# Optimization experiments

Hardware: AMD Instinct MI355X
Metric: run time of the kernel (lower is better)

The kernel has to match this reference:

```python
import jax, jax.numpy as jnp
import numpy as np

PRED_LEN = 24
F, I, H = 64, 128, 512  # features_size, input_size, hidden_size
B, S = 1024, 168        # batch, seq_len


def setup_inputs() -> dict:
    key = jax.random.key(0)
    ks = jax.random.split(key, 14)
    s = 0.05
    return {
        "x": jax.random.normal(ks[0], (B, S, F), dtype=jnp.float32),
        "W_enc": jax.random.normal(ks[1], (I, F), dtype=jnp.float32) * s,
        "b_enc": jax.random.normal(ks[2], (I,), dtype=jnp.float32) * s,
        "Wih0": jax.random.normal(ks[3], (4 * H, I), dtype=jnp.float32) * s,
        "Whh0": jax.random.normal(ks[4], (4 * H, H), dtype=jnp.float32) * s,
        "bih0": jax.random.normal(ks[5], (4 * H,), dtype=jnp.float32) * s,
        "bhh0": jax.random.normal(ks[6], (4 * H,), dtype=jnp.float32) * s,
        "Wih1": jax.random.normal(ks[7], (4 * H, H), dtype=jnp.float32) * s,
        "Whh1": jax.random.normal(ks[8], (4 * H, H), dtype=jnp.float32) * s,
        "bih1": jax.random.normal(ks[9], (4 * H,), dtype=jnp.float32) * s,
        "bhh1": jax.random.normal(ks[10], (4 * H,), dtype=jnp.float32) * s,
        "W_dec": jax.random.normal(ks[11], (F, H), dtype=jnp.float32) * s,
        "b_dec": jax.random.normal(ks[12], (F,), dtype=jnp.float32) * s,
    }


def _lstm_cell(xt, h, c, Wih, Whh, bih, bhh):
    # PyTorch gate order: i, f, g, o
    gates = xt @ Wih.T + h @ Whh.T + (bih + bhh)
    i, f, g, o = jnp.split(gates, 4, axis=-1)
    c = jax.nn.sigmoid(f) * c + jax.nn.sigmoid(i) * jnp.tanh(g)
    h = jax.nn.sigmoid(o) * jnp.tanh(c)
    return h, c


def reference(x, W_enc, b_enc, Wih0, Whh0, bih0, bhh0,
              Wih1, Whh1, bih1, bhh1, W_dec, b_dec):
    batch = x.shape[0]
    h0 = jnp.zeros((batch, H), x.dtype)
    init = (h0, h0, h0, h0)  # (h_l0, c_l0, h_l1, c_l1)

    def step(carry, xt):
        hl0, cl0, hl1, cl1 = carry
        enc = xt @ W_enc.T + b_enc
        hl0, cl0 = _lstm_cell(enc, hl0, cl0, Wih0, Whh0, bih0, bhh0)
        hl1, cl1 = _lstm_cell(hl0, hl1, cl1, Wih1, Whh1, bih1, bhh1)
        out = hl1 @ W_dec.T + b_dec
        return (hl0, cl0, hl1, cl1), out

    # teacher-forced pass over the observed sequence; keep only last output
    carry, outs = jax.lax.scan(step, init, jnp.transpose(x, (1, 0, 2)))
    last = outs[-1]  # [B, F], prediction for step seq_len (idx = seq_len-1)

    def ar_step(state, _):
        carry, prev = state
        carry, out = step(carry, prev)
        return (carry, out), out

    _, ar_outs = jax.lax.scan(ar_step, (carry, last), None, length=PRED_LEN - 1)
    outputs = jnp.concatenate([last[None], ar_outs], axis=0)  # [pred_len, B, F]
    return jnp.transpose(outputs, (1, 0, 2))  # [B, pred_len, F]
```

## Files before the change

### kernel.cpp

```cpp
#include <hip/hip_runtime.h>

#define B_   1024
#define S_   168
#define F_   64
#define I_   128
#define H_   512
#define G4   2048
#define PRED 24

typedef unsigned short u16;
typedef unsigned int   u32;
typedef __attribute__((ext_vector_type(8))) __bf16 bf16x8;
typedef __attribute__((ext_vector_type(4))) float  f32x4;
typedef __attribute__((ext_vector_type(4))) int    i32x4;

__device__ __forceinline__ u16 f2bf(float f) {
  u32 u = __float_as_uint(f);
  u += 0x7fff + ((u >> 16) & 1);
  return (u16)(u >> 16);
}
__device__ __forceinline__ float bf2f(u16 h) {
  return __uint_as_float(((u32)h) << 16);
}
__device__ __forceinline__ float sigm(float x) {
  x = fminf(fmaxf(x, -30.f), 30.f);
  return 1.f / (1.f + __expf(-x));
}
__device__ __forceinline__ float tanh_(float x) {
  x = fminf(fmaxf(x, -15.f), 15.f);
  float e = __expf(2.f * x);
  return (e - 1.f) / (e + 1.f);
}


__global__ void k_split(const float* __restrict__ src, u16* __restrict__ hi,
                        u16* __restrict__ lo, int n) {
  for (int i = blockIdx.x * 256 + threadIdx.x; i < n; i += gridDim.x * 256) {
    float a = src[i];
    u16 h = f2bf(a);
    hi[i] = h;
    lo[i] = f2bf(a - bf2f(h));
  }
}

__global__ void k_w0c(const float* __restrict__ Wih0, const float* __restrict__ Wenc,
                      float* __restrict__ W0c) {
  int id = blockIdx.x * 256 + threadIdx.x;
  int j = id >> 6, f = id & 63;
  float s = 0.f;
  for (int i = 0; i < 128; ++i) s += Wih0[j * 128 + i] * Wenc[i * 64 + f];
  W0c[id] = s;
}

__global__ void k_w0cd(const float* __restrict__ W0c, const float* __restrict__ Wdec,
                       float* __restrict__ W0cd) {
  int id = blockIdx.x * 256 + threadIdx.x;
  int j = id >> 9, m = id & 511;
  float s = 0.f;
  for (int f = 0; f < 64; ++f) s += W0c[j * 64 + f] * Wdec[f * 512 + m];
  W0cd[id] = s;
}

__global__ void k_biases(const float* __restrict__ Wih0, const float* __restrict__ benc,
                         const float* __restrict__ bih0, const float* __restrict__ bhh0,
                         const float* __restrict__ bih1, const float* __restrict__ bhh1,
                         float* __restrict__ b0c, float* __restrict__ b1c) {
  int j = blockIdx.x * 256 + threadIdx.x;
  float s = 0.f;
  for (int i = 0; i < 128; ++i) s += Wih0[j * 128 + i] * benc[i];
  b0c[j] = s + bih0[j] + bhh0[j];
  b1c[j] = bih1[j] + bhh1[j];
}

__global__ void k_b0ar(const float* __restrict__ W0c, const float* __restrict__ bdec,
                       const float* __restrict__ b0c, float* __restrict__ b0ar) {
  int j = blockIdx.x * 256 + threadIdx.x;
  float s = 0.f;
  for (int f = 0; f < 64; ++f) s += W0c[j * 64 + f] * bdec[f];
  b0ar[j] = b0c[j] + s;
}

__global__ void k_pack(const float* __restrict__ W, int K, u16* __restrict__ dst) {
  int id = blockIdx.x * 256 + threadIdx.x;
  int lane = id & 63, fi = id >> 6;
  int NK = K >> 5;
  int kt = fi % NK, jg = fi / NK;
  int g = jg & 3, jt = jg >> 2;
  int j = jt * 16 + (lane & 15);
  int kb = kt * 32 + (lane >> 4) * 8;
  const float* src = W + (size_t)(g * 512 + j) * K + kb;
  u16 hi[8] __attribute__((aligned(16)));
  u16 lo[8] __attribute__((aligned(16)));
#pragma unroll
  for (int e = 0; e < 8; ++e) {
    float v = src[e];
    u16 h = f2bf(v);
    hi[e] = h;
    lo[e] = f2bf(v - bf2f(h));
  }
  u16* d = dst + (size_t)fi * 1024 + lane * 8;
  *(i32x4*)d = *(const i32x4*)hi;
  *(i32x4*)(d + 512) = *(const i32x4*)lo;
}

__global__ __launch_bounds__(512, 2) void lstm3(
    const u16* __restrict__ A1hi, const u16* __restrict__ A1lo, int strideA1, int K1,
    const u16* __restrict__ W1p,
    const u16* __restrict__ A2hi, const u16* __restrict__ A2lo,
    const u16* __restrict__ W2p,
    const float* __restrict__ bias,
    float* __restrict__ c,
    u16* __restrict__ hhi, u16* __restrict__ hlo)
{
  __shared__ __align__(16) u16 smem_[49152];

  const int t = threadIdx.x;
  const int jblk = blockIdx.x, mblk = blockIdx.y;
  const int mbase = mblk * 64;
  const int lane = t & 63, wv = t >> 6;
  const int kk = wv >> 1, jh = wv & 1;
  const int lr = lane & 15, qk = lane >> 4;
  const int jtg = jblk * 2 + jh;
  const int nc1 = (K1 == 64) ? 1 : 4;
  const int NC  = nc1 + 4;
  const int NK1 = K1 >> 5;

  f32x4 acc[4][4];
#pragma unroll
  for (int mi = 0; mi < 4; ++mi)
#pragma unroll
    for (int g = 0; g < 4; ++g) acc[mi][g] = (f32x4){0.f, 0.f, 0.f, 0.f};

  auto prm = [&](int cc, const u16*& Ah, const u16*& Al, int& st, int& kb, int& Kc,
                 const u16*& Wp, int& NK) {
    if (cc < nc1) { Ah = A1hi; Al = A1lo; st = strideA1; kb = cc * 128;
                    Kc = (K1 == 64) ? 64 : 128; Wp = W1p; NK = NK1; }
    else { int i = cc - nc1; Ah = A2hi; Al = A2lo; st = 512; kb = i * 128;
           Kc = 128; Wp = W2p; NK = 16; }
  };
  auto nsof = [&](int cc) { return (cc < nc1 && K1 == 64) ? 2 : 4; };

  auto stageLoad = [&](int cc, i32x4* rr) {
    const u16 *Ah, *Al, *Wp_; int st, kb, Kc, NK;
    prm(cc, Ah, Al, st, kb, Kc, Wp_, NK);
    const int ppr = Kc >> 3;
    const int npc = (Kc == 128) ? 4 : 2;
#pragma unroll 4
    for (int p = 0; p < npc; ++p) {
      int li   = p * 512 + t;
      int part = li >= 64 * ppr;
      int liw  = li - part * 64 * ppr;
      int rown = (ppr == 16) ? (liw >> 4) : (liw >> 3);
      int kp   = liw & (ppr - 1);
      const u16* src = (part ? Al : Ah) + (size_t)(mbase + rown) * st + kb + kp * 8;
      rr[p] = *(const i32x4*)src;
    }
  };
  auto stageWrite = [&](int cc, const i32x4* rr, int buf) {
    const int Kc  = (cc < nc1 && K1 == 64) ? 64 : 128;
    const int ppr = Kc >> 3;
    const int npc = (Kc == 128) ? 4 : 2;
    u16* sb = smem_ + buf * 16384;
#pragma unroll 4
    for (int p = 0; p < npc; ++p) {
      int li   = p * 512 + t;
      int part = li >= 64 * ppr;
      int liw  = li - part * 64 * ppr;
      int rown = (ppr == 16) ? (liw >> 4) : (liw >> 3);
      int kp   = liw & (ppr - 1);
      *(i32x4*)&sb[(((part * 64 + rown) * ppr) + (kp ^ (rown & (ppr - 1)))) * 8] = rr[p];
    }
  };
  auto loadW = [&](const u16* Wp_, int NK, int kt, i32x4* wh, i32x4* wl) {
#pragma unroll
    for (int g = 0; g < 4; ++g) {
      const u16* p = Wp_ + (size_t)((jtg * 4 + g) * NK + kt) * 1024 + lane * 8;
      wh[g] = *(const i32x4*)p;
      wl[g] = *(const i32x4*)(p + 512);
    }
  };
  auto mstep = [&](int buf, int ppr, const i32x4* wh, const i32x4* wl) {
    const u16* sb = smem_ + buf * 16384;
    bf16x8 ah[4], al[4];
#pragma unroll
    for (int mi = 0; mi < 4; ++mi) {
      int rowA = mi * 16 + lr;
      int pl   = (kk * 4 + qk) ^ (rowA & (ppr - 1));
      ah[mi] = *(const bf16x8*)&sb[(rowA * ppr + pl) * 8];
      al[mi] = *(const bf16x8*)&sb[((64 + rowA) * ppr + pl) * 8];
    }
#pragma unroll
    for (int g = 0; g < 4; ++g) {
      bf16x8 bh = __builtin_bit_cast(bf16x8, wh[g]);
      bf16x8 bl = __builtin_bit_cast(bf16x8, wl[g]);
#pragma unroll
      for (int mi = 0; mi < 4; ++mi) {
        acc[mi][g] = __builtin_amdgcn_mfma_f32_16x16x32_bf16(ah[mi], bh, acc[mi][g], 0, 0, 0);
        acc[mi][g] = __builtin_amdgcn_mfma_f32_16x16x32_bf16(al[mi], bh, acc[mi][g], 0, 0, 0);
        acc[mi][g] = __builtin_amdgcn_mfma_f32_16x16x32_bf16(ah[mi], bl, acc[mi][g], 0, 0, 0);
      }
    }
  };

  i32x4 sreg[4];
  i32x4 whA[4], wlA[4], whB[4], wlB[4];

  stageLoad(0, sreg);
  stageWrite(0, sreg, 0);
  {
    const u16 *Ah, *Al, *Wp_; int st, kb, Kc, NK;
    prm(0, Ah, Al, st, kb, Kc, Wp_, NK);
    if (kk < nsof(0)) loadW(Wp_, NK, (kb >> 5) + kk, whA, wlA);
  }
  __syncthreads();

  for (int cc = 0; cc < NC; ++cc) {
    const int buf  = cc & 1;
    const bool more = (cc + 1 < NC);
    if (more) {
      stageLoad(cc + 1, sreg);
      const u16 *Ah, *Al, *Wp_; int st, kb, Kc, NK;
      prm(cc + 1, Ah, Al, st, kb, Kc, Wp_, NK);
      if (kk < nsof(cc + 1)) loadW(Wp_, NK, (kb >> 5) + kk, whB, wlB);
    }
    {
      const u16 *Ah, *Al, *Wp_; int st, kb, Kc, NK;
      prm(cc, Ah, Al, st, kb, Kc, Wp_, NK);
      if (kk < nsof(cc)) mstep(buf, Kc >> 3, whA, wlA);
    }
    if (more) stageWrite(cc + 1, sreg, buf ^ 1);
    __syncthreads();
    if (more) {
#pragma unroll
      for (int g = 0; g < 4; ++g) { whA[g] = whB[g]; wlA[g] = wlB[g]; }
    }
  }

  float* red = (float*)smem_;
#pragma unroll
  for (int mi = 0; mi < 4; ++mi) {
    if (mi != kk) {
      int slot = kk - (kk > mi ? 1 : 0);
      float* base = red + (size_t)(((jh * 4 + mi) * 3 + slot) * 1024) + lane * 4;
#pragma unroll
      for (int g = 0; g < 4; ++g) *(f32x4*)(base + g * 256) = acc[mi][g];
    }
  }
  __syncthreads();

  f32x4 r[4];
#pragma unroll
  for (int g = 0; g < 4; ++g) r[g] = acc[0][g];
  if (kk == 1) {
#pragma unroll
    for (int g = 0; g < 4; ++g) r[g] = acc[1][g];
  } else if (kk == 2) {
#pragma unroll
    for (int g = 0; g < 4; ++g) r[g] = acc[2][g];
  } else if (kk == 3) {
#pragma unroll
    for (int g = 0; g < 4; ++g) r[g] = acc[3][g];
  }
#pragma unroll
  for (int s = 0; s < 3; ++s) {
    float* base = red + (size_t)(((jh * 4 + kk) * 3 + s) * 1024) + lane * 4;
#pragma unroll
    for (int g = 0; g < 4; ++g) r[g] += *(const f32x4*)(base + g * 256);
  }

  const int   j   = jblk * 32 + jh * 16 + lr;
  const float bi  = bias[j];
  const float bff = bias[512 + j];
  const float bg  = bias[1024 + j];
  const float bo  = bias[1536 + j];
#pragma unroll
  for (int rr = 0; rr < 4; ++rr) {
    int b   = mbase + kk * 16 + qk * 4 + rr;
    int idx = b * 512 + j;
    float iv = sigm(r[0][rr] + bi);
    float fv = sigm(r[1][rr] + bff);
    float gv = tanh_(r[2][rr] + bg);
    float ov = sigm(r[3][rr] + bo);
    float cn = fv * c[idx] + iv * gv;
    c[idx] = cn;
    float hn = ov * tanh_(cn);
    u16 hh = f2bf(hn);
    hhi[idx] = hh;
    hlo[idx] = f2bf(hn - bf2f(hh));
  }
}

__global__ __launch_bounds__(256) void k_decoder(
    const u16* __restrict__ hhi, const u16* __restrict__ hlo,
    const float* __restrict__ Wdec, const float* __restrict__ bdec,
    float* __restrict__ out)
{
  __shared__ float sH[64][65];
  const int t = threadIdx.x;
  const int bbase = blockIdx.x * 64;
  const int mbase = blockIdx.y * 64;
  {
    int b = bbase + (t >> 2);
#pragma unroll
    for (int v = 0; v < 2; ++v) {
      int m0 = (t & 3) * 16 + v * 8;
      i32x4 hv = *(const i32x4*)&hhi[b * 512 + mbase + m0];
      i32x4 lv = *(const i32x4*)&hlo[b * 512 + mbase + m0];
      const u16* hp = (const u16*)&hv;
      const u16* lp = (const u16*)&lv;
#pragma unroll
      for (int e = 0; e < 8; ++e)
        sH[t >> 2][m0 + e] = bf2f(hp[e]) + bf2f(lp[e]);
    }
  }
  __syncthreads();
  const int bl = t & 63;
  const int wv = t >> 6;
  float acc[16];
#pragma unroll
  for (int u = 0; u < 16; ++u) acc[u] = 0.f;
  for (int m = 0; m < 64; ++m) {
    float hv = sH[bl][m];
#pragma unroll
    for (int u = 0; u < 16; ++u)
      acc[u] += hv * Wdec[(u * 4 + wv) * 512 + mbase + m];
  }
#pragma unroll
  for (int u = 0; u < 16; ++u) {
    int f = u * 4 + wv;
    float v = acc[u];
    if (blockIdx.y == 0) v += bdec[f];
    atomicAdd(&out[(bbase + bl) * (PRED * F_) + f], v);
  }
}


extern "C" void kernel_launch(void* const* d_in, const int* in_sizes, int n_in,
                              void* d_out, int out_size, void* d_ws, size_t ws_size,
                              hipStream_t stream) {
  const float* x    = (const float*)d_in[0];
  const float* Wenc = (const float*)d_in[1];
  const float* benc = (const float*)d_in[2];
  const float* Wih0 = (const float*)d_in[3];
  const float* Whh0 = (const float*)d_in[4];
  const float* bih0 = (const float*)d_in[5];
  const float* bhh0 = (const float*)d_in[6];
  const float* Wih1 = (const float*)d_in[7];
  const float* Whh1 = (const float*)d_in[8];
  const float* bih1 = (const float*)d_in[9];
  const float* bhh1 = (const float*)d_in[10];
  const float* Wdec = (const float*)d_in[11];
  const float* bdec = (const float*)d_in[12];
  float* out = (float*)d_out;

  char* p = (char*)d_ws;
  auto carve = [&](size_t bytes) { char* r = p; p += (bytes + 255) & ~(size_t)255; return r; };
  const size_t NX = (size_t)B_ * S_ * F_;
  const size_t NH = (size_t)B_ * H_;
  const size_t WP512 = (size_t)G4 * 512 * 2;
  u16* Xhi    = (u16*)carve(NX * 2);
  u16* Xlo    = (u16*)carve(NX * 2);
  float* W0c  = (float*)carve((size_t)G4 * 64 * 4);
  float* W0cd = (float*)carve((size_t)G4 * 512 * 4);
  u16* W0cp   = (u16*)carve((size_t)G4 * 64 * 2 * 2);
  u16* W0cdp  = (u16*)carve(WP512 * 2);
  u16* Whh0p  = (u16*)carve(WP512 * 2);
  u16* Wih1p  = (u16*)carve(WP512 * 2);
  u16* Whh1p  = (u16*)carve(WP512 * 2);
  float* b0c  = (float*)carve(G4 * 4);
  float* b0ar = (float*)carve(G4 * 4);
  float* b1c  = (float*)carve(G4 * 4);
  u16* h0hi[2] = {(u16*)carve(NH * 2), (u16*)carve(NH * 2)};
  u16* h0lo[2] = {(u16*)carve(NH * 2), (u16*)carve(NH * 2)};
  u16* h1hi[2] = {(u16*)carve(NH * 2), (u16*)carve(NH * 2)};
  u16* h1lo[2] = {(u16*)carve(NH * 2), (u16*)carve(NH * 2)};
  float* c0 = (float*)carve(NH * 4);
  float* c1 = (float*)carve(NH * 4);
  (void)ws_size; (void)n_in; (void)in_sizes;

  hipMemsetAsync(d_out, 0, (size_t)out_size * 4, stream);
  hipMemsetAsync(h0hi[0], 0, NH * 2, stream);
  hipMemsetAsync(h0lo[0], 0, NH * 2, stream);
  hipMemsetAsync(h1hi[0], 0, NH * 2, stream);
  hipMemsetAsync(h1lo[0], 0, NH * 2, stream);
  hipMemsetAsync(c0, 0, NH * 4, stream);
  hipMemsetAsync(c1, 0, NH * 4, stream);

  k_split<<<4096, 256, 0, stream>>>(x, Xhi, Xlo, (int)NX);
  k_w0c<<<512, 256, 0, stream>>>(Wih0, Wenc, W0c);
  k_w0cd<<<4096, 256, 0, stream>>>(W0c, Wdec, W0cd);
  k_biases<<<8, 256, 0, stream>>>(Wih0, benc, bih0, bhh0, bih1, bhh1, b0c, b1c);
  k_b0ar<<<8, 256, 0, stream>>>(W0c, bdec, b0c, b0ar);
  k_pack<<<32 * 16, 256, 0, stream>>>(Whh0, 512, Whh0p);
  k_pack<<<32 * 16, 256, 0, stream>>>(Wih1, 512, Wih1p);
  k_pack<<<32 * 16, 256, 0, stream>>>(Whh1, 512, Whh1p);
  k_pack<<<32 * 16, 256, 0, stream>>>(W0cd, 512, W0cdp);
  k_pack<<<32 * 2, 256, 0, stream>>>(W0c, 64, W0cp);

  dim3 grid(16, 16);
  for (int s = 0; s < S_ + PRED - 1; ++s) {
    int pp = s & 1, np = 1 - pp;
    if (s < S_) {
      lstm3<<<grid, 512, 0, stream>>>(
          Xhi + (size_t)s * F_, Xlo + (size_t)s * F_, S_ * F_, 64, W0cp,
          h0hi[pp], h0lo[pp], Whh0p,
          b0c, c0, h0hi[np], h0lo[np]);
    } else {
      lstm3<<<grid, 512, 0, stream>>>(
          h1hi[pp], h1lo[pp], 512, 512, W0cdp,
          h0hi[pp], h0lo[pp], Whh0p,
          b0ar, c0, h0hi[np], h0lo[np]);
    }
    lstm3<<<grid, 512, 0, stream>>>(
        h0hi[np], h0lo[np], 512, 512, Wih1p,
        h1hi[pp], h1lo[pp], Whh1p,
        b1c, c1, h1hi[np], h1lo[np]);
    if (s >= S_ - 1) {
      k_decoder<<<dim3(16, 8), 256, 0, stream>>>(
          h1hi[np], h1lo[np], Wdec, bdec, out + (size_t)(s - (S_ - 1)) * F_);
    }
  }
}
```

Measured before the change: 8.833 ms.

## Replace per-step kernel launches with a persistent cooperative LSTM kernel

Replaces the roughly 380 separate per-timestep lstm3 and decoder launches with one cooperative persistent kernel of 256 workgroups that loops over all timesteps. Grid-wide atomic-counter barriers separate the layer passes. Hidden states are interleaved as packed hi/lo bf16 pairs in u32 and read and written with agent-scope atomics, so the barriers can order them. The decoder is folded into the persistent loop. This removes launch overhead and inter-kernel gaps, at the cost of spin-barrier latency and of uncached atomic loads for the activations.

```diff
diff --git a/kernel.cpp b/kernel.cpp
--- a/kernel.cpp
+++ b/kernel.cpp
@@ -3,10 +3,11 @@
 #define B_   1024
 #define S_   168
 #define F_   64
-#define I_   128
 #define H_   512
 #define G4   2048
 #define PRED 24
+#define NWG  256
+#define NTH  512
 
 typedef unsigned short u16;
 typedef unsigned int   u32;
@@ -19,9 +20,7 @@
   u += 0x7fff + ((u >> 16) & 1);
   return (u16)(u >> 16);
 }
-__device__ __forceinline__ float bf2f(u16 h) {
-  return __uint_as_float(((u32)h) << 16);
-}
+__device__ __forceinline__ float bf2f(u16 h) { return __uint_as_float(((u32)h) << 16); }
 __device__ __forceinline__ float sigm(float x) {
   x = fminf(fmaxf(x, -30.f), 30.f);
   return 1.f / (1.f + __expf(-x));
@@ -33,13 +32,12 @@
 }
 
 
-__global__ void k_split(const float* __restrict__ src, u16* __restrict__ hi,
-                        u16* __restrict__ lo, int n) {
+__global__ void k_splitpack(const float* __restrict__ src, u32* __restrict__ dst, int n) {
   for (int i = blockIdx.x * 256 + threadIdx.x; i < n; i += gridDim.x * 256) {
     float a = src[i];
     u16 h = f2bf(a);
-    hi[i] = h;
-    lo[i] = f2bf(a - bf2f(h));
+    u16 l = f2bf(a - bf2f(h));
+    dst[i] = (u32)h | ((u32)l << 16);
   }
 }
 
@@ -103,234 +101,283 @@
   *(i32x4*)(d + 512) = *(const i32x4*)lo;
 }
 
-__global__ __launch_bounds__(512, 2) void lstm3(
-    const u16* __restrict__ A1hi, const u16* __restrict__ A1lo, int strideA1, int K1,
-    const u16* __restrict__ W1p,
-    const u16* __restrict__ A2hi, const u16* __restrict__ A2lo,
-    const u16* __restrict__ W2p,
-    const float* __restrict__ bias,
-    float* __restrict__ c,
-    u16* __restrict__ hhi, u16* __restrict__ hlo)
-{
-  __shared__ __align__(16) u16 smem_[49152];
+
+struct Params {
+  const u32* Xp;
+  const u16 *W0cp, *W0cdp, *Whh0p, *Wih1p, *Whh1p;
+  const float *b0c, *b0ar, *b1c;
+  u32 *h0a, *h0b, *h1a, *h1b;
+  float *c0, *c1;
+  const float *Wdec, *bdec;
+  float* out;
+  u32* cnt;
+};
+
+__global__ __launch_bounds__(NTH, 2) void lstm_persist(Params P) {
+  __shared__ __align__(16) u32 smem_[24576];
 
   const int t = threadIdx.x;
-  const int jblk = blockIdx.x, mblk = blockIdx.y;
+  const int wg = blockIdx.x;
+  const int jblk = wg & 15, mblk = wg >> 4;
   const int mbase = mblk * 64;
   const int lane = t & 63, wv = t >> 6;
   const int kk = wv >> 1, jh = wv & 1;
   const int lr = lane & 15, qk = lane >> 4;
   const int jtg = jblk * 2 + jh;
-  const int nc1 = (K1 == 64) ? 1 : 4;
-  const int NC  = nc1 + 4;
-  const int NK1 = K1 >> 5;
-
-  f32x4 acc[4][4];
-#pragma unroll
-  for (int mi = 0; mi < 4; ++mi)
-#pragma unroll
-    for (int g = 0; g < 4; ++g) acc[mi][g] = (f32x4){0.f, 0.f, 0.f, 0.f};
-
-  auto prm = [&](int cc, const u16*& Ah, const u16*& Al, int& st, int& kb, int& Kc,
-                 const u16*& Wp, int& NK) {
-    if (cc < nc1) { Ah = A1hi; Al = A1lo; st = strideA1; kb = cc * 128;
-                    Kc = (K1 == 64) ? 64 : 128; Wp = W1p; NK = NK1; }
-    else { int i = cc - nc1; Ah = A2hi; Al = A2lo; st = 512; kb = i * 128;
-           Kc = 128; Wp = W2p; NK = 16; }
+
+  u32 v[16];
+  i32x4 whA[4], wlA[4], whB[4], wlB[4];
+
+  auto gbar = [&](int tgt) {
+    __syncthreads();
+    if (t == 0) {
+      __hip_atomic_fetch_add(P.cnt, 1u, __ATOMIC_RELEASE, __HIP_MEMORY_SCOPE_AGENT);
+      while ((int)__hip_atomic_load(P.cnt, __ATOMIC_RELAXED, __HIP_MEMORY_SCOPE_AGENT) < tgt)
+        __builtin_amdgcn_s_sleep(1);
+    }
+    __syncthreads();
   };
-  auto nsof = [&](int cc) { return (cc < nc1 && K1 == 64) ? 2 : 4; };
-
-  auto stageLoad = [&](int cc, i32x4* rr) {
-    const u16 *Ah, *Al, *Wp_; int st, kb, Kc, NK;
-    prm(cc, Ah, Al, st, kb, Kc, Wp_, NK);
-    const int ppr = Kc >> 3;
-    const int npc = (Kc == 128) ? 4 : 2;
-#pragma unroll 4
-    for (int p = 0; p < npc; ++p) {
-      int li   = p * 512 + t;
-      int part = li >= 64 * ppr;
-      int liw  = li - part * 64 * ppr;
-      int rown = (ppr == 16) ? (liw >> 4) : (liw >> 3);
-      int kp   = liw & (ppr - 1);
-      const u16* src = (part ? Al : Ah) + (size_t)(mbase + rown) * st + kb + kp * 8;
-      rr[p] = *(const i32x4*)src;
+
+  auto layer_pass = [&](const u32* A1, int st1, int K1, const u16* W1p, bool a1u,
+                        const u32* A2, const u16* W2p,
+                        const float* bias, float* cmem, u32* hout) {
+    const int nc1 = (K1 == 64) ? 1 : 4;
+    const int NC  = nc1 + 4;
+    const int NK1 = K1 >> 5;
+
+    f32x4 acc[4][4];
+#pragma unroll
+    for (int mi = 0; mi < 4; ++mi)
+#pragma unroll
+      for (int g = 0; g < 4; ++g) acc[mi][g] = (f32x4){0.f, 0.f, 0.f, 0.f};
+
+    auto chunkKc = [&](int cc) { return (cc < nc1 && K1 == 64) ? 64 : 128; };
+    auto prmA = [&](int cc, const u32*& A, int& st, int& kb, bool& unc,
+                    const u16*& Wp, int& NK) {
+      if (cc < nc1) { A = A1; st = st1; kb = cc * 128; unc = a1u; Wp = W1p; NK = NK1; }
+      else { A = A2; st = 512; kb = (cc - nc1) * 128; unc = true; Wp = W2p; NK = 16; }
+    };
+
+    auto stage_load = [&](int cc) {
+      const u32* A; int st, kb; bool unc; const u16* Wp; int NK;
+      prmA(cc, A, st, kb, unc, Wp, NK);
+      if (chunkKc(cc) == 128) {
+        int rb = t >> 7, col = t & 127;
+        const u32* base = A + (size_t)(mbase + rb) * st + kb + col;
+        if (unc) {
+#pragma unroll
+          for (int i = 0; i < 16; ++i)
+            v[i] = __hip_atomic_load(base + (size_t)i * 4 * st, __ATOMIC_RELAXED,
+                                     __HIP_MEMORY_SCOPE_AGENT);
+        } else {
+#pragma unroll
+          for (int i = 0; i < 16; ++i) v[i] = base[(size_t)i * 4 * st];
+        }
+      } else {
+        int rb = t >> 6, col = t & 63;
+        const u32* base = A + (size_t)(mbase + rb) * st + kb + col;
+        if (unc) {
+#pragma unroll
+          for (int i = 0; i < 8; ++i)
+            v[i] = __hip_atomic_load(base + (size_t)i * 8 * st, __ATOMIC_RELAXED,
+                                     __HIP_MEMORY_SCOPE_AGENT);
+        } else {
+#pragma unroll
+          for (int i = 0; i < 8; ++i) v[i] = base[(size_t)i * 8 * st];
+        }
+      }
+    };
+
+    auto stage_write = [&](int cc, int buf) {
+      u32* sb = smem_ + buf * 8192;
+      if (chunkKc(cc) == 128) {
+        int rb = t >> 7, col = t & 127;
+        int pcol = col >> 3, e = col & 7;
+#pragma unroll
+        for (int i = 0; i < 16; ++i) {
+          int row = i * 4 + rb;
+          sb[row * 128 + (pcol ^ (row & 15)) * 8 + e] = v[i];
+        }
+      } else {
+        int rb = t >> 6, col = t & 63;
+        int pcol = col >> 3, e = col & 7;
+#pragma unroll
+        for (int i = 0; i < 8; ++i) {
+          int row = i * 8 + rb;
+          sb[row * 64 + (pcol ^ (row & 7)) * 8 + e] = v[i];
+        }
+      }
+    };
+
+    auto loadW = [&](const u16* Wp, int NK, int kt, i32x4* wh, i32x4* wl) {
+#pragma unroll
+      for (int g = 0; g < 4; ++g) {
+        const u16* p_ = Wp + (size_t)((jtg * 4 + g) * NK + kt) * 1024 + lane * 8;
+        wh[g] = *(const i32x4*)p_;
+        wl[g] = *(const i32x4*)(p_ + 512);
+      }
+    };
+
+    auto mstep = [&](int buf, int Kc) {
+      const u32* sb = smem_ + buf * 8192;
+      const int pm = (Kc >> 3) - 1;
+      bf16x8 ah[4], al[4];
+#pragma unroll
+      for (int mi = 0; mi < 4; ++mi) {
+        int rowA = mi * 16 + lr;
+        int pw = (kk * 4 + qk) ^ (rowA & pm);
+        const u32* pp_ = sb + rowA * Kc + pw * 8;
+        i32x4 d0 = *(const i32x4*)pp_;
+        i32x4 d1 = *(const i32x4*)(pp_ + 4);
+        i32x4 hv = { (int)__builtin_amdgcn_perm((u32)d0[1], (u32)d0[0], 0x05040100),
+                     (int)__builtin_amdgcn_perm((u32)d0[3], (u32)d0[2], 0x05040100),
+                     (int)__builtin_amdgcn_perm((u32)d1[1], (u32)d1[0], 0x05040100),
+                     (int)__builtin_amdgcn_perm((u32)d1[3], (u32)d1[2], 0x05040100) };
+        i32x4 lv = { (int)__builtin_amdgcn_perm((u32)d0[1], (u32)d0[0], 0x07060302),
+                     (int)__builtin_amdgcn_perm((u32)d0[3], (u32)d0[2], 0x07060302),
+                     (int)__builtin_amdgcn_perm((u32)d1[1], (u32)d1[0], 0x07060302),
+                     (int)__builtin_amdgcn_perm((u32)d1[3], (u32)d1[2], 0x07060302) };
+        ah[mi] = __builtin_bit_cast(bf16x8, hv);
+        al[mi] = __builtin_bit_cast(bf16x8, lv);
+      }
+#pragma unroll
+      for (int g = 0; g < 4; ++g) {
+        bf16x8 bh = __builtin_bit_cast(bf16x8, whA[g]);
+        bf16x8 bl = __builtin_bit_cast(bf16x8, wlA[g]);
+#pragma unroll
+        for (int mi = 0; mi < 4; ++mi) {
+          acc[mi][g] = __builtin_amdgcn_mfma_f32_16x16x32_bf16(ah[mi], bh, acc[mi][g], 0, 0, 0);
+          acc[mi][g] = __builtin_amdgcn_mfma_f32_16x16x32_bf16(al[mi], bh, acc[mi][g], 0, 0, 0);
+          acc[mi][g] = __builtin_amdgcn_mfma_f32_16x16x32_bf16(ah[mi], bl, acc[mi][g], 0, 0, 0);
+        }
+      }
+    };
+
+    stage_load(0);
+    stage_write(0, 0);
+    {
+      const u32* A; int st, kb; bool unc; const u16* Wp; int NK;
+      prmA(0, A, st, kb, unc, Wp, NK);
+      if (kk < (chunkKc(0) >> 5)) loadW(Wp, NK, (kb >> 5) + kk, whA, wlA);
+    }
+    __syncthreads();
+
+    for (int cc = 0; cc < NC; ++cc) {
+      int buf = cc & 1;
+      bool more = cc + 1 < NC;
+      if (more) {
+        stage_load(cc + 1);
+        const u32* A; int st, kb; bool unc; const u16* Wp; int NK;
+        prmA(cc + 1, A, st, kb, unc, Wp, NK);
+        if (kk < (chunkKc(cc + 1) >> 5)) loadW(Wp, NK, (kb >> 5) + kk, whB, wlB);
+      }
+      if (kk < (chunkKc(cc) >> 5)) mstep(buf, chunkKc(cc));
+      if (more) stage_write(cc + 1, buf ^ 1);
+      __syncthreads();
+      if (more) {
+#pragma unroll
+        for (int g = 0; g < 4; ++g) { whA[g] = whB[g]; wlA[g] = wlB[g]; }
+      }
+    }
+
+    float* red = (float*)smem_;
+#pragma unroll
+    for (int mi = 0; mi < 4; ++mi) {
+      if (mi != kk) {
+        int slot = kk - (kk > mi ? 1 : 0);
+        float* base = red + (size_t)(((jh * 4 + mi) * 3 + slot) * 1024) + lane * 4;
+#pragma unroll
+        for (int g = 0; g < 4; ++g) *(f32x4*)(base + g * 256) = acc[mi][g];
+      }
+    }
+    __syncthreads();
+
+    f32x4 r[4];
+#pragma unroll
+    for (int g = 0; g < 4; ++g) r[g] = acc[0][g];
+    if (kk == 1) {
+#pragma unroll
+      for (int g = 0; g < 4; ++g) r[g] = acc[1][g];
+    } else if (kk == 2) {
+#pragma unroll
+      for (int g = 0; g < 4; ++g) r[g] = acc[2][g];
+    } else if (kk == 3) {
+#pragma unroll
+      for (int g = 0; g < 4; ++g) r[g] = acc[3][g];
+    }
+#pragma unroll
+    for (int sl = 0; sl < 3; ++sl) {
+      float* base = red + (size_t)(((jh * 4 + kk) * 3 + sl) * 1024) + lane * 4;
+#pragma unroll
+      for (int g = 0; g < 4; ++g) r[g] += *(const f32x4*)(base + g * 256);
+    }
+
+    const int   j   = jblk * 32 + jh * 16 + lr;
+    const float bi  = bias[j];
+    const float bff = bias[512 + j];
+    const float bg  = bias[1024 + j];
+    const float bo  = bias[1536 + j];
+#pragma unroll
+    for (int rr = 0; rr < 4; ++rr) {
+      int b   = mbase + kk * 16 + qk * 4 + rr;
+      int idx = b * 512 + j;
+      float iv = sigm(r[0][rr] + bi);
+      float fv = sigm(r[1][rr] + bff);
+      float gv = tanh_(r[2][rr] + bg);
+      float ov = sigm(r[3][rr] + bo);
+      float cn = fv * cmem[idx] + iv * gv;
+      cmem[idx] = cn;
+      float hn = ov * tanh_(cn);
+      u16 hh = f2bf(hn);
+      u16 hl = f2bf(hn - bf2f(hh));
+      u32 hp = (u32)hh | ((u32)hl << 16);
+      __hip_atomic_store(&hout[idx], hp, __ATOMIC_RELAXED, __HIP_MEMORY_SCOPE_AGENT);
     }
   };
-  auto stageWrite = [&](int cc, const i32x4* rr, int buf) {
-    const int Kc  = (cc < nc1 && K1 == 64) ? 64 : 128;
-    const int ppr = Kc >> 3;
-    const int npc = (Kc == 128) ? 4 : 2;
-    u16* sb = smem_ + buf * 16384;
-#pragma unroll 4
-    for (int p = 0; p < npc; ++p) {
-      int li   = p * 512 + t;
-      int part = li >= 64 * ppr;
-      int liw  = li - part * 64 * ppr;
-      int rown = (ppr == 16) ? (liw >> 4) : (liw >> 3);
-      int kp   = liw & (ppr - 1);
-      *(i32x4*)&sb[(((part * 64 + rown) * ppr) + (kp ^ (rown & (ppr - 1)))) * 8] = rr[p];
-    }
-  };
-  auto loadW = [&](const u16* Wp_, int NK, int kt, i32x4* wh, i32x4* wl) {
-#pragma unroll
-    for (int g = 0; g < 4; ++g) {
-      const u16* p = Wp_ + (size_t)((jtg * 4 + g) * NK + kt) * 1024 + lane * 8;
-      wh[g] = *(const i32x4*)p;
-      wl[g] = *(const i32x4*)(p + 512);
-    }
-  };
-  auto mstep = [&](int buf, int ppr, const i32x4* wh, const i32x4* wl) {
-    const u16* sb = smem_ + buf * 16384;
-    bf16x8 ah[4], al[4];
-#pragma unroll
-    for (int mi = 0; mi < 4; ++mi) {
-      int rowA = mi * 16 + lr;
-      int pl   = (kk * 4 + qk) ^ (rowA & (ppr - 1));
-      ah[mi] = *(const bf16x8*)&sb[(rowA * ppr + pl) * 8];
-      al[mi] = *(const bf16x8*)&sb[((64 + rowA) * ppr + pl) * 8];
-    }
-#pragma unroll
-    for (int g = 0; g < 4; ++g) {
-      bf16x8 bh = __builtin_bit_cast(bf16x8, wh[g]);
-      bf16x8 bl = __builtin_bit_cast(bf16x8, wl[g]);
-#pragma unroll
-      for (int mi = 0; mi < 4; ++mi) {
-        acc[mi][g] = __builtin_amdgcn_mfma_f32_16x16x32_bf16(ah[mi], bh, acc[mi][g], 0, 0, 0);
-        acc[mi][g] = __builtin_amdgcn_mfma_f32_16x16x32_bf16(al[mi], bh, acc[mi][g], 0, 0, 0);
-        acc[mi][g] = __builtin_amdgcn_mfma_f32_16x16x32_bf16(ah[mi], bl, acc[mi][g], 0, 0, 0);
-      }
-    }
-  };
-
-  i32x4 sreg[4];
-  i32x4 whA[4], wlA[4], whB[4], wlB[4];
-
-  stageLoad(0, sreg);
-  stageWrite(0, sreg, 0);
-  {
-    const u16 *Ah, *Al, *Wp_; int st, kb, Kc, NK;
-    prm(0, Ah, Al, st, kb, Kc, Wp_, NK);
-    if (kk < nsof(0)) loadW(Wp_, NK, (kb >> 5) + kk, whA, wlA);
-  }
-  __syncthreads();
-
-  for (int cc = 0; cc < NC; ++cc) {
-    const int buf  = cc & 1;
-    const bool more = (cc + 1 < NC);
-    if (more) {
-      stageLoad(cc + 1, sreg);
-      const u16 *Ah, *Al, *Wp_; int st, kb, Kc, NK;
-      prm(cc + 1, Ah, Al, st, kb, Kc, Wp_, NK);
-      if (kk < nsof(cc + 1)) loadW(Wp_, NK, (kb >> 5) + kk, whB, wlB);
-    }
-    {
-      const u16 *Ah, *Al, *Wp_; int st, kb, Kc, NK;
-      prm(cc, Ah, Al, st, kb, Kc, Wp_, NK);
-      if (kk < nsof(cc)) mstep(buf, Kc >> 3, whA, wlA);
-    }
-    if (more) stageWrite(cc + 1, sreg, buf ^ 1);
-    __syncthreads();
-    if (more) {
-#pragma unroll
-      for (int g = 0; g < 4; ++g) { whA[g] = whB[g]; wlA[g] = wlB[g]; }
-    }
-  }
-
-  float* red = (float*)smem_;
-#pragma unroll
-  for (int mi = 0; mi < 4; ++mi) {
-    if (mi != kk) {
-      int slot = kk - (kk > mi ? 1 : 0);
-      float* base = red + (size_t)(((jh * 4 + mi) * 3 + slot) * 1024) + lane * 4;
-#pragma unroll
-      for (int g = 0; g < 4; ++g) *(f32x4*)(base + g * 256) = acc[mi][g];
-    }
-  }
-  __syncthreads();
-
-  f32x4 r[4];
-#pragma unroll
-  for (int g = 0; g < 4; ++g) r[g] = acc[0][g];
-  if (kk == 1) {
-#pragma unroll
-    for (int g = 0; g < 4; ++g) r[g] = acc[1][g];
-  } else if (kk == 2) {
-#pragma unroll
-    for (int g = 0; g < 4; ++g) r[g] = acc[2][g];
-  } else if (kk == 3) {
-#pragma unroll
-    for (int g = 0; g < 4; ++g) r[g] = acc[3][g];
-  }
-#pragma unroll
-  for (int s = 0; s < 3; ++s) {
-    float* base = red + (size_t)(((jh * 4 + kk) * 3 + s) * 1024) + lane * 4;
-#pragma unroll
-    for (int g = 0; g < 4; ++g) r[g] += *(const f32x4*)(base + g * 256);
-  }
-
-  const int   j   = jblk * 32 + jh * 16 + lr;
-  const float bi  = bias[j];
-  const float bff = bias[512 + j];
-  const float bg  = bias[1024 + j];
-  const float bo  = bias[1536 + j];
-#pragma unroll
-  for (int rr = 0; rr < 4; ++rr) {
-    int b   = mbase + kk * 16 + qk * 4 + rr;
-    int idx = b * 512 + j;
-    float iv = sigm(r[0][rr] + bi);
-    float fv = sigm(r[1][rr] + bff);
-    float gv = tanh_(r[2][rr] + bg);
-    float ov = sigm(r[3][rr] + bo);
-    float cn = fv * c[idx] + iv * gv;
-    c[idx] = cn;
-    float hn = ov * tanh_(cn);
-    u16 hh = f2bf(hn);
-    hhi[idx] = hh;
-    hlo[idx] = f2bf(hn - bf2f(hh));
-  }
-}
-
-__global__ __launch_bounds__(256) void k_decoder(
-    const u16* __restrict__ hhi, const u16* __restrict__ hlo,
-    const float* __restrict__ Wdec, const float* __restrict__ bdec,
-    float* __restrict__ out)
-{
-  __shared__ float sH[64][65];
-  const int t = threadIdx.x;
-  const int bbase = blockIdx.x * 64;
-  const int mbase = blockIdx.y * 64;
-  {
-    int b = bbase + (t >> 2);
-#pragma unroll
-    for (int v = 0; v < 2; ++v) {
-      int m0 = (t & 3) * 16 + v * 8;
-      i32x4 hv = *(const i32x4*)&hhi[b * 512 + mbase + m0];
-      i32x4 lv = *(const i32x4*)&hlo[b * 512 + mbase + m0];
-      const u16* hp = (const u16*)&hv;
-      const u16* lp = (const u16*)&lv;
-#pragma unroll
-      for (int e = 0; e < 8; ++e)
-        sH[t >> 2][m0 + e] = bf2f(hp[e]) + bf2f(lp[e]);
-    }
-  }
-  __syncthreads();
-  const int bl = t & 63;
-  const int wv = t >> 6;
-  float acc[16];
-#pragma unroll
-  for (int u = 0; u < 16; ++u) acc[u] = 0.f;
-  for (int m = 0; m < 64; ++m) {
-    float hv = sH[bl][m];
-#pragma unroll
-    for (int u = 0; u < 16; ++u)
-      acc[u] += hv * Wdec[(u * 4 + wv) * 512 + mbase + m];
-  }
-#pragma unroll
-  for (int u = 0; u < 16; ++u) {
-    int f = u * 4 + wv;
-    float v = acc[u];
-    if (blockIdx.y == 0) v += bdec[f];
-    atomicAdd(&out[(bbase + bl) * (PRED * F_) + f], v);
+
+  int target = 0;
+  u32 *h0r = P.h0a, *h0w = P.h0b, *h1r = P.h1a, *h1w = P.h1b;
+
+  for (int s = 0; s < S_ + PRED - 1; ++s) {
+    if (s < S_)
+      layer_pass(P.Xp + (size_t)s * F_, S_ * F_, 64, P.W0cp, false,
+                 h0r, P.Whh0p, P.b0c, P.c0, h0w);
+    else
+      layer_pass(h1r, 512, 512, P.W0cdp, true,
+                 h0r, P.Whh0p, P.b0ar, P.c0, h0w);
+    gbar(target += NWG);
+
+    layer_pass(h0w, 512, 512, P.Wih1p, true,
+               h1r, P.Whh1p, P.b1c, P.c1, h1w);
+    gbar(target += NWG);
+
+    if (s >= S_ - 1) {
+      float* outp = P.out + (size_t)(s - (S_ - 1)) * F_;
+      int bb = mblk * 64 + (t >> 3);
+      int k0 = jblk * 32;
+      int f0 = (t & 7) * 8;
+      float a[8];
+#pragma unroll
+      for (int ff = 0; ff < 8; ++ff) a[ff] = 0.f;
+      for (int k = 0; k < 32; ++k) {
+        u32 pk = __hip_atomic_load(&h1w[(size_t)bb * 512 + k0 + k], __ATOMIC_RELAXED,
+                                   __HIP_MEMORY_SCOPE_AGENT);
+        float hv = bf2f((u16)(pk & 0xffffu)) + bf2f((u16)(pk >> 16));
+#pragma unroll
+        for (int ff = 0; ff < 8; ++ff)
+          a[ff] += hv * P.Wdec[(f0 + ff) * 512 + k0 + k];
+      }
+#pragma unroll
+      for (int ff = 0; ff < 8; ++ff) {
+        float vv = a[ff];
+        if (k0 == 0) vv += P.bdec[f0 + ff];
+        atomicAdd(&outp[(size_t)bb * (PRED * F_) + f0 + ff], vv);
+      }
+    }
+
+    u32* tmp;
+    tmp = h0r; h0r = h0w; h0w = tmp;
+    tmp = h1r; h1r = h1w; h1w = tmp;
   }
 }
 
@@ -351,42 +398,40 @@
   const float* bhh1 = (const float*)d_in[10];
   const float* Wdec = (const float*)d_in[11];
   const float* bdec = (const float*)d_in[12];
-  float* out = (float*)d_out;
 
   char* p = (char*)d_ws;
   auto carve = [&](size_t bytes) { char* r = p; p += (bytes + 255) & ~(size_t)255; return r; };
   const size_t NX = (size_t)B_ * S_ * F_;
   const size_t NH = (size_t)B_ * H_;
-  const size_t WP512 = (size_t)G4 * 512 * 2;
-  u16* Xhi    = (u16*)carve(NX * 2);
-  u16* Xlo    = (u16*)carve(NX * 2);
+  const size_t WPK = (size_t)G4 * 512 * 2 * 2;
+  u32* Xp     = (u32*)carve(NX * 4);
   float* W0c  = (float*)carve((size_t)G4 * 64 * 4);
   float* W0cd = (float*)carve((size_t)G4 * 512 * 4);
   u16* W0cp   = (u16*)carve((size_t)G4 * 64 * 2 * 2);
-  u16* W0cdp  = (u16*)carve(WP512 * 2);
-  u16* Whh0p  = (u16*)carve(WP512 * 2);
-  u16* Wih1p  = (u16*)carve(WP512 * 2);
-  u16* Whh1p  = (u16*)carve(WP512 * 2);
+  u16* W0cdp  = (u16*)carve(WPK);
+  u16* Whh0p  = (u16*)carve(WPK);
+  u16* Wih1p  = (u16*)carve(WPK);
+  u16* Whh1p  = (u16*)carve(WPK);
   float* b0c  = (float*)carve(G4 * 4);
   float* b0ar = (float*)carve(G4 * 4);
   float* b1c  = (float*)carve(G4 * 4);
-  u16* h0hi[2] = {(u16*)carve(NH * 2), (u16*)carve(NH * 2)};
-  u16* h0lo[2] = {(u16*)carve(NH * 2), (u16*)carve(NH * 2)};
-  u16* h1hi[2] = {(u16*)carve(NH * 2), (u16*)carve(NH * 2)};
-  u16* h1lo[2] = {(u16*)carve(NH * 2), (u16*)carve(NH * 2)};
+  u32* h0a = (u32*)carve(NH * 4);
+  u32* h0b = (u32*)carve(NH * 4);
+  u32* h1a = (u32*)carve(NH * 4);
+  u32* h1b = (u32*)carve(NH * 4);
   float* c0 = (float*)carve(NH * 4);
   float* c1 = (float*)carve(NH * 4);
+  u32* cnt  = (u32*)carve(256);
   (void)ws_size; (void)n_in; (void)in_sizes;
 
   hipMemsetAsync(d_out, 0, (size_t)out_size * 4, stream);
-  hipMemsetAsync(h0hi[0], 0, NH * 2, stream);
-  hipMemsetAsync(h0lo[0], 0, NH * 2, stream);
-  hipMemsetAsync(h1hi[0], 0, NH * 2, stream);
-  hipMemsetAsync(h1lo[0], 0, NH * 2, stream);
+  hipMemsetAsync(h0a, 0, NH * 4, stream);
+  hipMemsetAsync(h1a, 0, NH * 4, stream);
   hipMemsetAsync(c0, 0, NH * 4, stream);
   hipMemsetAsync(c1, 0, NH * 4, stream);
-
-  k_split<<<4096, 256, 0, stream>>>(x, Xhi, Xlo, (int)NX);
+  hipMemsetAsync(cnt, 0, 256, stream);
+
+  k_splitpack<<<4096, 256, 0, stream>>>(x, Xp, (int)NX);
   k_w0c<<<512, 256, 0, stream>>>(Wih0, Wenc, W0c);
   k_w0cd<<<4096, 256, 0, stream>>>(W0c, Wdec, W0cd);
   k_biases<<<8, 256, 0, stream>>>(Wih0, benc, bih0, bhh0, bih1, bhh1, b0c, b1c);
@@ -397,27 +442,18 @@
   k_pack<<<32 * 16, 256, 0, stream>>>(W0cd, 512, W0cdp);
   k_pack<<<32 * 2, 256, 0, stream>>>(W0c, 64, W0cp);
 
-  dim3 grid(16, 16);
-  for (int s = 0; s < S_ + PRED - 1; ++s) {
-    int pp = s & 1, np = 1 - pp;
-    if (s < S_) {
-      lstm3<<<grid, 512, 0, stream>>>(
-          Xhi + (size_t)s * F_, Xlo + (size_t)s * F_, S_ * F_, 64, W0cp,
-          h0hi[pp], h0lo[pp], Whh0p,
-          b0c, c0, h0hi[np], h0lo[np]);
-    } else {
-      lstm3<<<grid, 512, 0, stream>>>(
-          h1hi[pp], h1lo[pp], 512, 512, W0cdp,
-          h0hi[pp], h0lo[pp], Whh0p,
-          b0ar, c0, h0hi[np], h0lo[np]);
-    }
-    lstm3<<<grid, 512, 0, stream>>>(
-        h0hi[np], h0lo[np], 512, 512, Wih1p,
-        h1hi[pp], h1lo[pp], Whh1p,
-        b1c, c1, h1hi[np], h1lo[np]);
-    if (s >= S_ - 1) {
-      k_decoder<<<dim3(16, 8), 256, 0, stream>>>(
-          h1hi[np], h1lo[np], Wdec, bdec, out + (size_t)(s - (S_ - 1)) * F_);
-    }
-  }
-}
+  Params prm;
+  prm.Xp = Xp;
+  prm.W0cp = W0cp; prm.W0cdp = W0cdp; prm.Whh0p = Whh0p;
+  prm.Wih1p = Wih1p; prm.Whh1p = Whh1p;
+  prm.b0c = b0c; prm.b0ar = b0ar; prm.b1c = b1c;
+  prm.h0a = h0a; prm.h0b = h0b; prm.h1a = h1a; prm.h1b = h1b;
+  prm.c0 = c0; prm.c1 = c1;
+  prm.Wdec = Wdec; prm.bdec = bdec;
+  prm.out = (float*)d_out;
+  prm.cnt = cnt;
+
+  void* kargs[] = { &prm };
+  hipLaunchCooperativeKernel(reinterpret_cast<void*>(lstm_persist),
+                             dim3(NWG), dim3(NTH), kargs, 0, stream);
+}
```

Result: slower. 17.06 ms (+93.1%).
